# Kernel tuning notes

Hardware: AMD Instinct MI355X
Metric: run time of the kernel (lower is better)

Reference implementation:

```python
import jax, jax.numpy as jnp
import numpy as np

N_NODES = 50000
N_EDGES = 800000
IN_DIM = 128
HIDDEN = 32
HEADS = 4
OUT_DIM = 64
NEG_SLOPE = 0.2  # PyG GATConv default


def setup_inputs() -> dict:
    key = jax.random.key(0)
    ks = jax.random.split(key, 12)
    s = 0.05
    return {
        "x": jax.random.normal(ks[0], (N_NODES, IN_DIM), dtype=jnp.float32),
        "edge_index": jax.random.randint(ks[1], (2, N_EDGES), 0, N_NODES, dtype=jnp.int64),
        # layer 1: out = HEADS * HIDDEN, concat=True
        "W1": jax.random.normal(ks[2], (IN_DIM, HEADS * HIDDEN), dtype=jnp.float32) * s,
        "a_src1": jax.random.normal(ks[3], (HEADS, HIDDEN), dtype=jnp.float32) * s,
        "a_dst1": jax.random.normal(ks[4], (HEADS, HIDDEN), dtype=jnp.float32) * s,
        "b1": jnp.zeros((HEADS * HIDDEN,), dtype=jnp.float32),
        # layer 2: heads=1, concat=False
        "W2": jax.random.normal(ks[5], (HEADS * HIDDEN, OUT_DIM), dtype=jnp.float32) * s,
        "a_src2": jax.random.normal(ks[6], (1, OUT_DIM), dtype=jnp.float32) * s,
        "a_dst2": jax.random.normal(ks[7], (1, OUT_DIM), dtype=jnp.float32) * s,
        "b2": jnp.zeros((OUT_DIM,), dtype=jnp.float32),
    }


def _gat_conv(x, src, dst, W, a_src, a_dst, b, heads, concat):
    """PyG-style GATConv. src/dst already include self-loops."""
    N = x.shape[0]
    C = W.shape[1] // heads
    h = (x @ W).reshape(N, heads, C)              # [N,H,C]
    al_s = jnp.sum(h * a_src, axis=-1)            # [N,H]
    al_d = jnp.sum(h * a_dst, axis=-1)            # [N,H]
    e = jax.nn.leaky_relu(al_s[src] + al_d[dst], NEG_SLOPE)  # [E,H]
    # numerically-stable segment softmax over incoming edges of each dst node
    m = jax.ops.segment_max(e, dst, num_segments=N)          # [N,H]
    ex = jnp.exp(e - m[dst])
    denom = jax.ops.segment_sum(ex, dst, num_segments=N)     # [N,H]
    alpha = ex / denom[dst]                                   # [E,H]
    out = jax.ops.segment_sum(h[src] * alpha[:, :, None], dst, num_segments=N)  # [N,H,C]
    out = out.reshape(N, heads * C) if concat else out.mean(axis=1)
    return out + b


def reference(x, edge_index, W1, a_src1, a_dst1, b1, W2, a_src2, a_dst2, b2):
    N = x.shape[0]
    loop = jnp.arange(N, dtype=edge_index.dtype)
    src = jnp.concatenate([edge_index[0], loop])
    dst = jnp.concatenate([edge_index[1], loop])
    h = jax.nn.relu(_gat_conv(x, src, dst, W1, a_src1, a_dst1, b1, HEADS, True))
    out = _gat_conv(h, src, dst, W2, a_src2, a_dst2, b2, 1, False)
    return jax.nn.log_softmax(out, axis=1)
```

## Files before the change

### kernel.cpp

```cpp
#include <hip/hip_runtime.h>
#include <hip/hip_bf16.h>
#include <math.h>

#define N_NODES 50000
#define N_EDGES 800000
#define E_TOT   (N_EDGES + N_NODES)
#define IN_DIM  128
#define HID     128
#define ODIM    64
#define NEG     0.2f
#define NB1     ((N_NODES + 255) / 256)
#define NCHUNK  ((N_NODES + 31) / 32)
#define NREP    8

typedef short bf16x8 __attribute__((ext_vector_type(8)));
typedef float f32x4 __attribute__((ext_vector_type(4)));
typedef float f32x2 __attribute__((ext_vector_type(2)));
typedef unsigned short ushort_t;

__device__ __forceinline__ float lrelu(float x) { return x >= 0.f ? x : NEG * x; }

__device__ __forceinline__ unsigned short f2b(float v) {
  unsigned int b = __float_as_uint(v);
  b += 0x7fffu + ((b >> 16) & 1u);
  return (unsigned short)(b >> 16);
}
__device__ __forceinline__ float b2f(unsigned short u) {
  return __uint_as_float(((unsigned int)u) << 16);
}
__device__ __forceinline__ unsigned int f2b2(float lo, float hi) {
  union { __hip_bfloat162 h; unsigned int u; } cv;
  cv.h = __float22bfloat162_rn(make_float2(lo, hi));
  return cv.u;
}
__device__ __forceinline__ float blo(unsigned int v) { return __uint_as_float(v << 16); }
__device__ __forceinline__ float bhi(unsigned int v) { return __uint_as_float(v & 0xffff0000u); }

__device__ __forceinline__ f32x2 f8x2lo(unsigned int v) {
  return __builtin_amdgcn_cvt_pk_f32_fp8((int)v, false);
}
__device__ __forceinline__ f32x2 f8x2hi(unsigned int v) {
  return __builtin_amdgcn_cvt_pk_f32_fp8((int)v, true);
}
__device__ __forceinline__ unsigned char f2f8(float v) {
  return (unsigned char)(__builtin_amdgcn_cvt_pk_fp8_f32(v, v, 0, false) & 0xff);
}

__device__ __forceinline__ int e_src(const void* ei, int f, int e) {
  if (e >= N_EDGES) return e - N_EDGES;
  return f ? (int)((const long long*)ei)[e] : ((const int*)ei)[e];
}
__device__ __forceinline__ int e_dst(const void* ei, int f, int e) {
  if (e >= N_EDGES) return e - N_EDGES;
  return f ? (int)((const long long*)ei)[N_EDGES + e] : ((const int*)ei)[N_EDGES + e];
}

__global__ void k_prep(const float* __restrict__ W1, const float* __restrict__ W2,
                       ushort_t* __restrict__ Wt1, ushort_t* __restrict__ Wt2,
                       const void* ei, int* flag) {
  if (blockIdx.x == 64) {
    if (threadIdx.x == 0) {
      const int* p = (const int*)ei;
      int allz = 1;
      for (int i = 0; i < 64; ++i) if (p[2 * i + 1] != 0) { allz = 0; break; }
      *flag = allz;
    }
    return;
  }
  int i = blockIdx.x * 256 + threadIdx.x;
  if (i < 128 * 128) { int k = i >> 7, n = i & 127; Wt1[n * 128 + k] = f2b(W1[i]); }
  if (i < 128 * 64)  { int k = i >> 6, n = i & 63;  Wt2[n * 128 + k] = f2b(W2[i]); }
}

__global__ void k_hist(const void* ei, const int* flag, int* degr, int* rank) {
  int e = blockIdx.x * 256 + threadIdx.x;
  if (e >= E_TOT) return;
  int r = blockIdx.x & (NREP - 1);
  int d = e_dst(ei, *flag, e);
  rank[e] = atomicAdd(&degr[r * N_NODES + d], 1);
}

__global__ void k_scan1(const int* __restrict__ degr, int* __restrict__ offs, int* __restrict__ bsums) {
  __shared__ int sm[256];
  int t = threadIdx.x, i = blockIdx.x * 256 + t;
  int v = 0;
  if (i < N_NODES) {
    #pragma unroll
    for (int r = 0; r < NREP; ++r) v += degr[r * N_NODES + i];
  }
  sm[t] = v;
  __syncthreads();
  for (int o = 1; o < 256; o <<= 1) {
    int add = (t >= o) ? sm[t - o] : 0;
    __syncthreads();
    sm[t] += add;
    __syncthreads();
  }
  if (i < N_NODES) offs[i] = sm[t] - v;
  if (t == 255) bsums[blockIdx.x] = sm[255];
}

__global__ void k_scan2(int* bsums) {
  __shared__ int sm[256];
  int t = threadIdx.x;
  int v = (t < NB1) ? bsums[t] : 0;
  sm[t] = v;
  __syncthreads();
  for (int o = 1; o < 256; o <<= 1) {
    int add = (t >= o) ? sm[t - o] : 0;
    __syncthreads();
    sm[t] += add;
    __syncthreads();
  }
  if (t < NB1) bsums[t] = sm[t] - v;
}

__global__ void k_scan3(int* __restrict__ offs, const int* __restrict__ bsums,
                        const int* __restrict__ degr, int* __restrict__ repbase) {
  int i = blockIdx.x * 256 + threadIdx.x;
  if (i < N_NODES) {
    int o = offs[i] + bsums[blockIdx.x];
    offs[i] = o;
    int run = o;
    #pragma unroll
    for (int r = 0; r < NREP; ++r) {
      repbase[r * N_NODES + i] = run;
      run += degr[r * N_NODES + i];
    }
  }
  if (i == 0) offs[N_NODES] = E_TOT;
}

__global__ void k_scatter(const void* ei, const int* __restrict__ flag,
                          const int* __restrict__ repbase,
                          const int* __restrict__ rank, int* __restrict__ srcs) {
  int e = blockIdx.x * 256 + threadIdx.x;
  if (e >= E_TOT) return;
  int f = *flag;
  int d = e_dst(ei, f, e);
  int r = blockIdx.x & (NREP - 1);
  srcs[repbase[r * N_NODES + d] + rank[e]] = e_src(ei, f, e);
}

__global__ __launch_bounds__(256) void k_mm1(const float* __restrict__ x,
                                             const ushort_t* __restrict__ Wt,
                                             ushort_t* __restrict__ h1b,
                                             unsigned char* __restrict__ h1f8) {
  __shared__ ushort_t xs[32 * 128];
  int t = threadIdx.x;
  int w = t >> 6, l = t & 63;
  int lr = l & 15, lk = l >> 4;
  int nodeSub = (w & 1) * 16, colBase = (w >> 1) * 64;
  bf16x8 bfrag[4][4];
  #pragma unroll
  for (int ct = 0; ct < 4; ++ct)
    #pragma unroll
    for (int ks = 0; ks < 4; ++ks) {
      int n = colBase + ct * 16 + lr;
      int k = ks * 32 + lk * 8;
      bfrag[ct][ks] = *(const bf16x8*)&Wt[n * 128 + k];
    }
  int rr = t >> 3, c0 = (t & 7) * 16;
  for (int chunk = blockIdx.x; chunk < NCHUNK; chunk += gridDim.x) {
    int base = chunk * 32;
    int srcRow = base + rr; if (srcRow >= N_NODES) srcRow = N_NODES - 1;
    const float4* xr = (const float4*)&x[(size_t)srcRow * IN_DIM + c0];
    float4 f0 = xr[0], f1 = xr[1], f2 = xr[2], f3 = xr[3];
    uint4 w0, w1;
    w0.x = f2b2(f0.x, f0.y); w0.y = f2b2(f0.z, f0.w);
    w0.z = f2b2(f1.x, f1.y); w0.w = f2b2(f1.z, f1.w);
    w1.x = f2b2(f2.x, f2.y); w1.y = f2b2(f2.z, f2.w);
    w1.z = f2b2(f3.x, f3.y); w1.w = f2b2(f3.z, f3.w);
    char* xsb = (char*)xs;
    int swz = (rr & 7) << 4;
    *(uint4*)(xsb + rr * 256 + ((c0 * 2 +  0) ^ swz)) = w0;
    *(uint4*)(xsb + rr * 256 + ((c0 * 2 + 16) ^ swz)) = w1;
    __syncthreads();
    f32x4 acc[4] = {{0,0,0,0},{0,0,0,0},{0,0,0,0},{0,0,0,0}};
    int arow = nodeSub + lr;
    #pragma unroll
    for (int ks = 0; ks < 4; ++ks) {
      bf16x8 a = *(const bf16x8*)((const char*)xs + arow * 256 +
                                  ((ks * 64 + lk * 16) ^ ((arow & 7) << 4)));
      #pragma unroll
      for (int ct = 0; ct < 4; ++ct)
        acc[ct] = __builtin_amdgcn_mfma_f32_16x16x32_bf16(a, bfrag[ct][ks], acc[ct], 0, 0, 0);
    }
    __syncthreads();
    #pragma unroll
    for (int ct = 0; ct < 4; ++ct)
      #pragma unroll
      for (int r = 0; r < 4; ++r) {
        int node = base + nodeSub + lk * 4 + r;
        if (node < N_NODES) {
          float v = acc[ct][r];
          int col = colBase + ct * 16 + lr;
          h1b[(size_t)node * HID + col] = f2b(v);
          h1f8[(size_t)node * HID + col] = f2f8(v);
        }
      }
  }
}

__global__ __launch_bounds__(256) void k_mm2(const ushort_t* __restrict__ xb,
                                             const ushort_t* __restrict__ Wt,
                                             ushort_t* __restrict__ h2b,
                                             unsigned char* __restrict__ h2f8) {
  __shared__ ushort_t xs[32 * 128];
  int t = threadIdx.x;
  int w = t >> 6, l = t & 63;
  int lr = l & 15, lk = l >> 4;
  int nodeSub = (w & 1) * 16, colBase = (w >> 1) * 32;
  bf16x8 bfrag[2][4];
  #pragma unroll
  for (int ct = 0; ct < 2; ++ct)
    #pragma unroll
    for (int ks = 0; ks < 4; ++ks) {
      int n = colBase + ct * 16 + lr;
      int k = ks * 32 + lk * 8;
      bfrag[ct][ks] = *(const bf16x8*)&Wt[n * 128 + k];
    }
  int rr = t >> 3, c0 = (t & 7) * 16;
  for (int chunk = blockIdx.x; chunk < NCHUNK; chunk += gridDim.x) {
    int base = chunk * 32;
    int srcRow = base + rr; if (srcRow >= N_NODES) srcRow = N_NODES - 1;
    const uint4* xr = (const uint4*)&xb[(size_t)srcRow * HID + c0];
    uint4 w0 = xr[0], w1 = xr[1];
    char* xsb = (char*)xs;
    int swz = (rr & 7) << 4;
    *(uint4*)(xsb + rr * 256 + ((c0 * 2 +  0) ^ swz)) = w0;
    *(uint4*)(xsb + rr * 256 + ((c0 * 2 + 16) ^ swz)) = w1;
    __syncthreads();
    f32x4 acc[2] = {{0,0,0,0},{0,0,0,0}};
    int arow = nodeSub + lr;
    #pragma unroll
    for (int ks = 0; ks < 4; ++ks) {
      bf16x8 a = *(const bf16x8*)((const char*)xs + arow * 256 +
                                  ((ks * 64 + lk * 16) ^ ((arow & 7) << 4)));
      #pragma unroll
      for (int ct = 0; ct < 2; ++ct)
        acc[ct] = __builtin_amdgcn_mfma_f32_16x16x32_bf16(a, bfrag[ct][ks], acc[ct], 0, 0, 0);
    }
    __syncthreads();
    #pragma unroll
    for (int ct = 0; ct < 2; ++ct)
      #pragma unroll
      for (int r = 0; r < 4; ++r) {
        int node = base + nodeSub + lk * 4 + r;
        if (node < N_NODES) {
          float v = acc[ct][r];
          int col = colBase + ct * 16 + lr;
          h2b[(size_t)node * ODIM + col] = f2b(v);
          h2f8[(size_t)node * ODIM + col] = f2f8(v);
        }
      }
  }
}

__global__ __launch_bounds__(256) void k_al1(const ushort_t* __restrict__ h1b,
                                             const float* __restrict__ asrc,
                                             const float* __restrict__ adst, float* __restrict__ als,
                                             float* __restrict__ ald) {
  int t = threadIdx.x;
  int n = blockIdx.x * 16 + (t >> 4);
  int c8 = (t & 15) * 8;
  uint4 v = *(const uint4*)&h1b[(size_t)n * HID + c8];
  float4 a0 = *(const float4*)&asrc[c8], a1 = *(const float4*)&asrc[c8 + 4];
  float4 d0 = *(const float4*)&adst[c8], d1 = *(const float4*)&adst[c8 + 4];
  float f0 = blo(v.x), f1 = bhi(v.x), f2 = blo(v.y), f3 = bhi(v.y);
  float f4 = blo(v.z), f5 = bhi(v.z), f6 = blo(v.w), f7 = bhi(v.w);
  float s = f0*a0.x + f1*a0.y + f2*a0.z + f3*a0.w + f4*a1.x + f5*a1.y + f6*a1.z + f7*a1.w;
  float d = f0*d0.x + f1*d0.y + f2*d0.z + f3*d0.w + f4*d1.x + f5*d1.y + f6*d1.z + f7*d1.w;
  s += __shfl_xor(s, 1); s += __shfl_xor(s, 2);
  d += __shfl_xor(d, 1); d += __shfl_xor(d, 2);
  if ((t & 3) == 0) {
    int head = (t & 15) >> 2;
    als[n * 4 + head] = s;
    ald[n * 4 + head] = d;
  }
}

__global__ __launch_bounds__(256) void k_al2(const ushort_t* __restrict__ h2b,
                                             const float* __restrict__ asrc,
                                             const float* __restrict__ adst, float* __restrict__ als,
                                             float* __restrict__ ald) {
  int t = threadIdx.x;
  int n = blockIdx.x * 32 + (t >> 3);
  if (n >= N_NODES) return;
  int c8 = (t & 7) * 8;
  uint4 v = *(const uint4*)&h2b[(size_t)n * ODIM + c8];
  float4 a0 = *(const float4*)&asrc[c8], a1 = *(const float4*)&asrc[c8 + 4];
  float4 d0 = *(const float4*)&adst[c8], d1 = *(const float4*)&adst[c8 + 4];
  float f0 = blo(v.x), f1 = bhi(v.x), f2 = blo(v.y), f3 = bhi(v.y);
  float f4 = blo(v.z), f5 = bhi(v.z), f6 = blo(v.w), f7 = bhi(v.w);
  float s = f0*a0.x + f1*a0.y + f2*a0.z + f3*a0.w + f4*a1.x + f5*a1.y + f6*a1.z + f7*a1.w;
  float d = f0*d0.x + f1*d0.y + f2*d0.z + f3*d0.w + f4*d1.x + f5*d1.y + f6*d1.z + f7*d1.w;
  s += __shfl_xor(s, 1); s += __shfl_xor(s, 2); s += __shfl_xor(s, 4);
  d += __shfl_xor(d, 1); d += __shfl_xor(d, 2); d += __shfl_xor(d, 4);
  if ((t & 7) == 0) { als[n] = s; ald[n] = d; }
}

__global__ __launch_bounds__(256) void k_agg1(const unsigned char* __restrict__ h1f8,
                                              const float* __restrict__ als,
                                              const float* __restrict__ ald, const int* __restrict__ offs,
                                              const int* __restrict__ srcs, const float* __restrict__ b1,
                                              ushort_t* __restrict__ out1b) {
  int t = threadIdx.x;
  int w = t >> 6, l = t & 63;
  int hw = l >> 5, lh = l & 31;
  int sg = lh >> 4, cl = lh & 15, head = cl >> 2;
  int lbase = hw << 5;
  int n = blockIdx.x * 8 + w * 2 + hw;
  int off0 = offs[n], deg = offs[n + 1] - off0;
  const float4* als4 = (const float4*)als;
  float4 ad = ((const float4*)ald)[n];
  const unsigned char* hb = h1f8 + cl * 8;

  float ds = 0.f;
  float num0 = 0, num1 = 0, num2 = 0, num3 = 0, num4 = 0, num5 = 0, num6 = 0, num7 = 0;

  for (int cbase = 0; cbase < deg; cbase += 32) {
    int j0 = cbase + lh;
    float w0 = 0.f, w1 = 0.f, w2 = 0.f, w3 = 0.f;
    int sb = 0;
    if (j0 < deg) {
      int s = srcs[off0 + j0];
      sb = s << 7;
      float4 a = als4[s];
      w0 = __expf(lrelu(a.x + ad.x)); w1 = __expf(lrelu(a.y + ad.y));
      w2 = __expf(lrelu(a.z + ad.z)); w3 = __expf(lrelu(a.w + ad.w));
    }
    int pw01 = (int)f2b2(w0, w1), pw23 = (int)f2b2(w2, w3);
    int cn = (deg - cbase) < 32 ? (deg - cbase) : 32;
    for (int jj = 0; jj < cn; jj += 4) {
      int jA = jj + sg, jB = jj + 2 + sg;
      int boA = __shfl(sb, lbase + jA), boB = __shfl(sb, lbase + jB);
      uint2 vA = *(const uint2*)(hb + boA);
      uint2 vB = *(const uint2*)(hb + boB);
      unsigned int uA01 = (unsigned int)__shfl(pw01, lbase + jA);
      unsigned int uA23 = (unsigned int)__shfl(pw23, lbase + jA);
      unsigned int uB01 = (unsigned int)__shfl(pw01, lbase + jB);
      unsigned int uB23 = (unsigned int)__shfl(pw23, lbase + jB);
      unsigned int upA = head < 2 ? uA01 : uA23;
      unsigned int upB = head < 2 ? uB01 : uB23;
      float wA = (head & 1) ? bhi(upA) : blo(upA);
      float wB = (head & 1) ? bhi(upB) : blo(upB);
      ds += wA + wB;
      f32x2 p0 = f8x2lo(vA.x), p1 = f8x2hi(vA.x);
      f32x2 p2 = f8x2lo(vA.y), p3 = f8x2hi(vA.y);
      num0 = fmaf(wA, p0.x, num0); num1 = fmaf(wA, p0.y, num1);
      num2 = fmaf(wA, p1.x, num2); num3 = fmaf(wA, p1.y, num3);
      num4 = fmaf(wA, p2.x, num4); num5 = fmaf(wA, p2.y, num5);
      num6 = fmaf(wA, p3.x, num6); num7 = fmaf(wA, p3.y, num7);
      p0 = f8x2lo(vB.x); p1 = f8x2hi(vB.x);
      p2 = f8x2lo(vB.y); p3 = f8x2hi(vB.y);
      num0 = fmaf(wB, p0.x, num0); num1 = fmaf(wB, p0.y, num1);
      num2 = fmaf(wB, p1.x, num2); num3 = fmaf(wB, p1.y, num3);
      num4 = fmaf(wB, p2.x, num4); num5 = fmaf(wB, p2.y, num5);
      num6 = fmaf(wB, p3.x, num6); num7 = fmaf(wB, p3.y, num7);
    }
  }
  num0 += __shfl_xor(num0, 16); num1 += __shfl_xor(num1, 16);
  num2 += __shfl_xor(num2, 16); num3 += __shfl_xor(num3, 16);
  num4 += __shfl_xor(num4, 16); num5 += __shfl_xor(num5, 16);
  num6 += __shfl_xor(num6, 16); num7 += __shfl_xor(num7, 16);
  ds += __shfl_xor(ds, 16);
  if (lh < 16) {
    float rd = 1.f / ds;
    int c8 = cl * 8;
    float4 bb0 = *(const float4*)&b1[c8];
    float4 bb1 = *(const float4*)&b1[c8 + 4];
    float o0 = fmaxf(num0 * rd + bb0.x, 0.f);
    float o1 = fmaxf(num1 * rd + bb0.y, 0.f);
    float o2 = fmaxf(num2 * rd + bb0.z, 0.f);
    float o3 = fmaxf(num3 * rd + bb0.w, 0.f);
    float o4 = fmaxf(num4 * rd + bb1.x, 0.f);
    float o5 = fmaxf(num5 * rd + bb1.y, 0.f);
    float o6 = fmaxf(num6 * rd + bb1.z, 0.f);
    float o7 = fmaxf(num7 * rd + bb1.w, 0.f);
    uint4 pk;
    pk.x = f2b2(o0, o1); pk.y = f2b2(o2, o3);
    pk.z = f2b2(o4, o5); pk.w = f2b2(o6, o7);
    *(uint4*)&out1b[(size_t)n * HID + c8] = pk;
  }
}

__global__ __launch_bounds__(256) void k_agg2(const unsigned char* __restrict__ h2f8,
                                              const float* __restrict__ als,
                                              const float* __restrict__ ald, const int* __restrict__ offs,
                                              const int* __restrict__ srcs, const float* __restrict__ b2,
                                              float* __restrict__ out) {
  int t = threadIdx.x;
  int w = t >> 6, l = t & 63;
  int hw = l >> 5, lh = l & 31;
  int sg = lh >> 3, cl = lh & 7;
  int lbase = hw << 5;
  int n = blockIdx.x * 8 + w * 2 + hw;
  int off0 = offs[n], deg = offs[n + 1] - off0;
  float adv = ald[n];
  const unsigned char* hb = h2f8 + cl * 8;

  float ds = 0.f;
  float num0 = 0, num1 = 0, num2 = 0, num3 = 0, num4 = 0, num5 = 0, num6 = 0, num7 = 0;

  for (int cbase = 0; cbase < deg; cbase += 32) {
    int j0 = cbase + lh;
    float wv = 0.f;
    int sb = 0;
    if (j0 < deg) {
      int s = srcs[off0 + j0];
      sb = s << 6;
      wv = __expf(lrelu(als[s] + adv));
    }
    int cn = (deg - cbase) < 32 ? (deg - cbase) : 32;
    for (int jj = 0; jj < cn; jj += 8) {
      int jA = jj + sg, jB = jj + 4 + sg;
      int boA = __shfl(sb, lbase + jA), boB = __shfl(sb, lbase + jB);
      uint2 vA = *(const uint2*)(hb + boA);
      uint2 vB = *(const uint2*)(hb + boB);
      float wA = __shfl(wv, lbase + jA), wB = __shfl(wv, lbase + jB);
      ds += wA + wB;
      f32x2 p0 = f8x2lo(vA.x), p1 = f8x2hi(vA.x);
      f32x2 p2 = f8x2lo(vA.y), p3 = f8x2hi(vA.y);
      num0 = fmaf(wA, p0.x, num0); num1 = fmaf(wA, p0.y, num1);
      num2 = fmaf(wA, p1.x, num2); num3 = fmaf(wA, p1.y, num3);
      num4 = fmaf(wA, p2.x, num4); num5 = fmaf(wA, p2.y, num5);
      num6 = fmaf(wA, p3.x, num6); num7 = fmaf(wA, p3.y, num7);
      p0 = f8x2lo(vB.x); p1 = f8x2hi(vB.x);
      p2 = f8x2lo(vB.y); p3 = f8x2hi(vB.y);
      num0 = fmaf(wB, p0.x, num0); num1 = fmaf(wB, p0.y, num1);
      num2 = fmaf(wB, p1.x, num2); num3 = fmaf(wB, p1.y, num3);
      num4 = fmaf(wB, p2.x, num4); num5 = fmaf(wB, p2.y, num5);
      num6 = fmaf(wB, p3.x, num6); num7 = fmaf(wB, p3.y, num7);
    }
  }
  #pragma unroll
  for (int o = 8; o <= 16; o <<= 1) {
    num0 += __shfl_xor(num0, o); num1 += __shfl_xor(num1, o);
    num2 += __shfl_xor(num2, o); num3 += __shfl_xor(num3, o);
    num4 += __shfl_xor(num4, o); num5 += __shfl_xor(num5, o);
    num6 += __shfl_xor(num6, o); num7 += __shfl_xor(num7, o);
    ds += __shfl_xor(ds, o);
  }
  if (lh < 8) {
    float rd = 1.f / ds;
    int c8 = cl * 8;
    float4 bb0 = *(const float4*)&b2[c8];
    float4 bb1 = *(const float4*)&b2[c8 + 4];
    float v0 = num0 * rd + bb0.x, v1 = num1 * rd + bb0.y;
    float v2 = num2 * rd + bb0.z, v3 = num3 * rd + bb0.w;
    float v4 = num4 * rd + bb1.x, v5 = num5 * rd + bb1.y;
    float v6 = num6 * rd + bb1.z, v7 = num7 * rd + bb1.w;
    float mx = fmaxf(fmaxf(fmaxf(v0, v1), fmaxf(v2, v3)), fmaxf(fmaxf(v4, v5), fmaxf(v6, v7)));
    #pragma unroll
    for (int o = 1; o <= 4; o <<= 1) mx = fmaxf(mx, __shfl_xor(mx, o));
    float sum = __expf(v0 - mx) + __expf(v1 - mx) + __expf(v2 - mx) + __expf(v3 - mx)
              + __expf(v4 - mx) + __expf(v5 - mx) + __expf(v6 - mx) + __expf(v7 - mx);
    #pragma unroll
    for (int o = 1; o <= 4; o <<= 1) sum += __shfl_xor(sum, o);
    float ls = __logf(sum);
    float4 r0, r1;
    r0.x = (v0 - mx) - ls; r0.y = (v1 - mx) - ls; r0.z = (v2 - mx) - ls; r0.w = (v3 - mx) - ls;
    r1.x = (v4 - mx) - ls; r1.y = (v5 - mx) - ls; r1.z = (v6 - mx) - ls; r1.w = (v7 - mx) - ls;
    *(float4*)&out[(size_t)n * ODIM + c8] = r0;
    *(float4*)&out[(size_t)n * ODIM + c8 + 4] = r1;
  }
}

extern "C" void kernel_launch(void* const* d_in, const int* in_sizes, int n_in,
                              void* d_out, int out_size, void* d_ws, size_t ws_size,
                              hipStream_t stream) {
  const float* x   = (const float*)d_in[0];
  const void*  ei  = d_in[1];
  const float* W1  = (const float*)d_in[2];
  const float* as1 = (const float*)d_in[3];
  const float* ad1 = (const float*)d_in[4];
  const float* b1  = (const float*)d_in[5];
  const float* W2  = (const float*)d_in[6];
  const float* as2 = (const float*)d_in[7];
  const float* ad2 = (const float*)d_in[8];
  const float* b2  = (const float*)d_in[9];
  float* out = (float*)d_out;

  char* ws = (char*)d_ws;
  size_t o = 0;
  auto alloc = [&](size_t bytes) { void* p = (void*)(ws + o); o += (bytes + 255) & ~(size_t)255; return p; };
  ushort_t* h1b   = (ushort_t*)alloc((size_t)N_NODES * HID * 2);
  ushort_t* out1b = (ushort_t*)alloc((size_t)N_NODES * HID * 2);
  ushort_t* h2b   = (ushort_t*)alloc((size_t)N_NODES * ODIM * 2);
  unsigned char* h1f8 = (unsigned char*)alloc((size_t)N_NODES * HID);
  ushort_t* Wt1   = (ushort_t*)alloc((size_t)128 * 128 * 2);
  ushort_t* Wt2   = (ushort_t*)alloc((size_t)64 * 128 * 2);
  float* als1 = (float*)alloc((size_t)N_NODES * 4 * 4);
  float* ald1 = (float*)alloc((size_t)N_NODES * 4 * 4);
  float* als2 = (float*)alloc((size_t)N_NODES * 4);
  float* ald2 = (float*)alloc((size_t)N_NODES * 4);
  int*   degr = (int*)alloc((size_t)NREP * N_NODES * 4);
  int*   repbase = (int*)alloc((size_t)NREP * N_NODES * 4);
  int*   offs = (int*)alloc((size_t)(N_NODES + 1) * 4);
  int*   rank = (int*)alloc((size_t)E_TOT * 4);
  int*   srcs = (int*)alloc((size_t)E_TOT * 4);
  int*   bsums= (int*)alloc((size_t)NB1 * 4);
  int*   flag = (int*)alloc(4);
  unsigned char* h2f8 = (unsigned char*)rank;

  hipMemsetAsync(degr, 0, (size_t)NREP * N_NODES * 4, stream);
  k_prep   <<<65,    256, 0, stream>>>(W1, W2, Wt1, Wt2, ei, flag);

  int egrid = (E_TOT + 255) / 256;
  k_hist   <<<egrid, 256, 0, stream>>>(ei, flag, degr, rank);
  k_scan1  <<<NB1,   256, 0, stream>>>(degr, offs, bsums);
  k_scan2  <<<1,     256, 0, stream>>>(bsums);
  k_scan3  <<<NB1,   256, 0, stream>>>(offs, bsums, degr, repbase);
  k_scatter<<<egrid, 256, 0, stream>>>(ei, flag, repbase, rank, srcs);

  k_mm1  <<<512, 256, 0, stream>>>(x, Wt1, h1b, h1f8);
  k_al1  <<<N_NODES / 16, 256, 0, stream>>>(h1b, as1, ad1, als1, ald1);
  k_agg1 <<<N_NODES / 8, 256, 0, stream>>>(h1f8, als1, ald1, offs, srcs, b1, out1b);

  k_mm2  <<<512, 256, 0, stream>>>(out1b, Wt2, h2b, h2f8);
  k_al2  <<<(N_NODES + 31) / 32, 256, 0, stream>>>(h2b, as2, ad2, als2, ald2);
  k_agg2 <<<N_NODES / 8, 256, 0, stream>>>(h2f8, als2, ald2, offs, srcs, b2, out);
}
```

Measured before the change: 134.3 us.

## Fold memset and scan2 into neighbours; drop shuffle staging in aggregation kernels

The degree-array memset moves into extra blocks of the prep kernel, and the single-block scan2 is removed by having each scan3 block reduce the preceding block sums itself. This cuts two launches from the serial chain. Both aggregation kernels also drop the cooperative load-then-shuffle scheme: each lane now loads its own source index and per-head attention logit and computes the exp weight directly. This removes the shuffles and bf16 weight packing but repeats the index loads and exp work across lanes.

```diff
diff --git a/kernel.cpp b/kernel.cpp
--- a/kernel.cpp
+++ b/kernel.cpp
@@ -57,7 +57,7 @@
 
 __global__ void k_prep(const float* __restrict__ W1, const float* __restrict__ W2,
                        ushort_t* __restrict__ Wt1, ushort_t* __restrict__ Wt2,
-                       const void* ei, int* flag) {
+                       const void* ei, int* flag, int4* __restrict__ degr4) {
   if (blockIdx.x == 64) {
     if (threadIdx.x == 0) {
       const int* p = (const int*)ei;
@@ -67,6 +67,11 @@
     }
     return;
   }
+  if (blockIdx.x > 64) {
+    int i = (blockIdx.x - 65) * 256 + threadIdx.x;
+    if (i < NREP * N_NODES / 4) degr4[i] = make_int4(0, 0, 0, 0);
+    return;
+  }
   int i = blockIdx.x * 256 + threadIdx.x;
   if (i < 128 * 128) { int k = i >> 7, n = i & 127; Wt1[n * 128 + k] = f2b(W1[i]); }
   if (i < 128 * 64)  { int k = i >> 6, n = i & 63;  Wt2[n * 128 + k] = f2b(W2[i]); }
@@ -100,26 +105,19 @@
   if (t == 255) bsums[blockIdx.x] = sm[255];
 }
 
-__global__ void k_scan2(int* bsums) {
-  __shared__ int sm[256];
-  int t = threadIdx.x;
-  int v = (t < NB1) ? bsums[t] : 0;
-  sm[t] = v;
-  __syncthreads();
-  for (int o = 1; o < 256; o <<= 1) {
-    int add = (t >= o) ? sm[t - o] : 0;
-    __syncthreads();
-    sm[t] += add;
-    __syncthreads();
-  }
-  if (t < NB1) bsums[t] = sm[t] - v;
-}
-
 __global__ void k_scan3(int* __restrict__ offs, const int* __restrict__ bsums,
                         const int* __restrict__ degr, int* __restrict__ repbase) {
-  int i = blockIdx.x * 256 + threadIdx.x;
+  __shared__ int red[4];
+  int t = threadIdx.x;
+  int v = (t < blockIdx.x) ? bsums[t] : 0;
+  #pragma unroll
+  for (int o = 32; o >= 1; o >>= 1) v += __shfl_xor(v, o);
+  if ((t & 63) == 0) red[t >> 6] = v;
+  __syncthreads();
+  int pre = red[0] + red[1] + red[2] + red[3];
+  int i = blockIdx.x * 256 + t;
   if (i < N_NODES) {
-    int o = offs[i] + bsums[blockIdx.x];
+    int o = offs[i] + pre;
     offs[i] = o;
     int run = o;
     #pragma unroll
@@ -309,56 +307,50 @@
   int w = t >> 6, l = t & 63;
   int hw = l >> 5, lh = l & 31;
   int sg = lh >> 4, cl = lh & 15, head = cl >> 2;
-  int lbase = hw << 5;
   int n = blockIdx.x * 8 + w * 2 + hw;
   int off0 = offs[n], deg = offs[n + 1] - off0;
-  const float4* als4 = (const float4*)als;
-  float4 ad = ((const float4*)ald)[n];
+  float adh = ald[n * 4 + head];
   const unsigned char* hb = h1f8 + cl * 8;
 
   float ds = 0.f;
   float num0 = 0, num1 = 0, num2 = 0, num3 = 0, num4 = 0, num5 = 0, num6 = 0, num7 = 0;
 
-  for (int cbase = 0; cbase < deg; cbase += 32) {
-    int j0 = cbase + lh;
-    float w0 = 0.f, w1 = 0.f, w2 = 0.f, w3 = 0.f;
-    int sb = 0;
-    if (j0 < deg) {
-      int s = srcs[off0 + j0];
-      sb = s << 7;
-      float4 a = als4[s];
-      w0 = __expf(lrelu(a.x + ad.x)); w1 = __expf(lrelu(a.y + ad.y));
-      w2 = __expf(lrelu(a.z + ad.z)); w3 = __expf(lrelu(a.w + ad.w));
-    }
-    int pw01 = (int)f2b2(w0, w1), pw23 = (int)f2b2(w2, w3);
-    int cn = (deg - cbase) < 32 ? (deg - cbase) : 32;
-    for (int jj = 0; jj < cn; jj += 4) {
-      int jA = jj + sg, jB = jj + 2 + sg;
-      int boA = __shfl(sb, lbase + jA), boB = __shfl(sb, lbase + jB);
-      uint2 vA = *(const uint2*)(hb + boA);
-      uint2 vB = *(const uint2*)(hb + boB);
-      unsigned int uA01 = (unsigned int)__shfl(pw01, lbase + jA);
-      unsigned int uA23 = (unsigned int)__shfl(pw23, lbase + jA);
-      unsigned int uB01 = (unsigned int)__shfl(pw01, lbase + jB);
-      unsigned int uB23 = (unsigned int)__shfl(pw23, lbase + jB);
-      unsigned int upA = head < 2 ? uA01 : uA23;
-      unsigned int upB = head < 2 ? uB01 : uB23;
-      float wA = (head & 1) ? bhi(upA) : blo(upA);
-      float wB = (head & 1) ? bhi(upB) : blo(upB);
-      ds += wA + wB;
-      f32x2 p0 = f8x2lo(vA.x), p1 = f8x2hi(vA.x);
-      f32x2 p2 = f8x2lo(vA.y), p3 = f8x2hi(vA.y);
-      num0 = fmaf(wA, p0.x, num0); num1 = fmaf(wA, p0.y, num1);
-      num2 = fmaf(wA, p1.x, num2); num3 = fmaf(wA, p1.y, num3);
-      num4 = fmaf(wA, p2.x, num4); num5 = fmaf(wA, p2.y, num5);
-      num6 = fmaf(wA, p3.x, num6); num7 = fmaf(wA, p3.y, num7);
-      p0 = f8x2lo(vB.x); p1 = f8x2hi(vB.x);
-      p2 = f8x2lo(vB.y); p3 = f8x2hi(vB.y);
-      num0 = fmaf(wB, p0.x, num0); num1 = fmaf(wB, p0.y, num1);
-      num2 = fmaf(wB, p1.x, num2); num3 = fmaf(wB, p1.y, num3);
-      num4 = fmaf(wB, p2.x, num4); num5 = fmaf(wB, p2.y, num5);
-      num6 = fmaf(wB, p3.x, num6); num7 = fmaf(wB, p3.y, num7);
-    }
+  int j = sg;
+  for (; j + 2 < deg; j += 4) {
+    int sA = srcs[off0 + j];
+    int sB = srcs[off0 + j + 2];
+    float aA = als[sA * 4 + head];
+    float aB = als[sB * 4 + head];
+    uint2 vA = *(const uint2*)(hb + (sA << 7));
+    uint2 vB = *(const uint2*)(hb + (sB << 7));
+    float wA = __expf(lrelu(aA + adh));
+    float wB = __expf(lrelu(aB + adh));
+    ds += wA + wB;
+    f32x2 p0 = f8x2lo(vA.x), p1 = f8x2hi(vA.x);
+    f32x2 p2 = f8x2lo(vA.y), p3 = f8x2hi(vA.y);
+    num0 = fmaf(wA, p0.x, num0); num1 = fmaf(wA, p0.y, num1);
+    num2 = fmaf(wA, p1.x, num2); num3 = fmaf(wA, p1.y, num3);
+    num4 = fmaf(wA, p2.x, num4); num5 = fmaf(wA, p2.y, num5);
+    num6 = fmaf(wA, p3.x, num6); num7 = fmaf(wA, p3.y, num7);
+    p0 = f8x2lo(vB.x); p1 = f8x2hi(vB.x);
+    p2 = f8x2lo(vB.y); p3 = f8x2hi(vB.y);
+    num0 = fmaf(wB, p0.x, num0); num1 = fmaf(wB, p0.y, num1);
+    num2 = fmaf(wB, p1.x, num2); num3 = fmaf(wB, p1.y, num3);
+    num4 = fmaf(wB, p2.x, num4); num5 = fmaf(wB, p2.y, num5);
+    num6 = fmaf(wB, p3.x, num6); num7 = fmaf(wB, p3.y, num7);
+  }
+  if (j < deg) {
+    int sA = srcs[off0 + j];
+    float aA = als[sA * 4 + head];
+    uint2 vA = *(const uint2*)(hb + (sA << 7));
+    float wA = __expf(lrelu(aA + adh));
+    ds += wA;
+    f32x2 p0 = f8x2lo(vA.x), p1 = f8x2hi(vA.x);
+    f32x2 p2 = f8x2lo(vA.y), p3 = f8x2hi(vA.y);
+    num0 = fmaf(wA, p0.x, num0); num1 = fmaf(wA, p0.y, num1);
+    num2 = fmaf(wA, p1.x, num2); num3 = fmaf(wA, p1.y, num3);
+    num4 = fmaf(wA, p2.x, num4); num5 = fmaf(wA, p2.y, num5);
+    num6 = fmaf(wA, p3.x, num6); num7 = fmaf(wA, p3.y, num7);
   }
   num0 += __shfl_xor(num0, 16); num1 += __shfl_xor(num1, 16);
   num2 += __shfl_xor(num2, 16); num3 += __shfl_xor(num3, 16);
@@ -394,7 +386,6 @@
   int w = t >> 6, l = t & 63;
   int hw = l >> 5, lh = l & 31;
   int sg = lh >> 3, cl = lh & 7;
-  int lbase = hw << 5;
   int n = blockIdx.x * 8 + w * 2 + hw;
   int off0 = offs[n], deg = offs[n + 1] - off0;
   float adv = ald[n];
@@ -403,36 +394,42 @@
   float ds = 0.f;
   float num0 = 0, num1 = 0, num2 = 0, num3 = 0, num4 = 0, num5 = 0, num6 = 0, num7 = 0;
 
-  for (int cbase = 0; cbase < deg; cbase += 32) {
-    int j0 = cbase + lh;
-    float wv = 0.f;
-    int sb = 0;
-    if (j0 < deg) {
-      int s = srcs[off0 + j0];
-      sb = s << 6;
-      wv = __expf(lrelu(als[s] + adv));
-    }
-    int cn = (deg - cbase) < 32 ? (deg - cbase) : 32;
-    for (int jj = 0; jj < cn; jj += 8) {
-      int jA = jj + sg, jB = jj + 4 + sg;
-      int boA = __shfl(sb, lbase + jA), boB = __shfl(sb, lbase + jB);
-      uint2 vA = *(const uint2*)(hb + boA);
-      uint2 vB = *(const uint2*)(hb + boB);
-      float wA = __shfl(wv, lbase + jA), wB = __shfl(wv, lbase + jB);
-      ds += wA + wB;
-      f32x2 p0 = f8x2lo(vA.x), p1 = f8x2hi(vA.x);
-      f32x2 p2 = f8x2lo(vA.y), p3 = f8x2hi(vA.y);
-      num0 = fmaf(wA, p0.x, num0); num1 = fmaf(wA, p0.y, num1);
-      num2 = fmaf(wA, p1.x, num2); num3 = fmaf(wA, p1.y, num3);
-      num4 = fmaf(wA, p2.x, num4); num5 = fmaf(wA, p2.y, num5);
-      num6 = fmaf(wA, p3.x, num6); num7 = fmaf(wA, p3.y, num7);
-      p0 = f8x2lo(vB.x); p1 = f8x2hi(vB.x);
-      p2 = f8x2lo(vB.y); p3 = f8x2hi(vB.y);
-      num0 = fmaf(wB, p0.x, num0); num1 = fmaf(wB, p0.y, num1);
-      num2 = fmaf(wB, p1.x, num2); num3 = fmaf(wB, p1.y, num3);
-      num4 = fmaf(wB, p2.x, num4); num5 = fmaf(wB, p2.y, num5);
-      num6 = fmaf(wB, p3.x, num6); num7 = fmaf(wB, p3.y, num7);
-    }
+  int j = sg;
+  for (; j + 4 < deg; j += 8) {
+    int sA = srcs[off0 + j];
+    int sB = srcs[off0 + j + 4];
+    float aA = als[sA];
+    float aB = als[sB];
+    uint2 vA = *(const uint2*)(hb + (sA << 6));
+    uint2 vB = *(const uint2*)(hb + (sB << 6));
+    float wA = __expf(lrelu(aA + adv));
+    float wB = __expf(lrelu(aB + adv));
+    ds += wA + wB;
+    f32x2 p0 = f8x2lo(vA.x), p1 = f8x2hi(vA.x);
+    f32x2 p2 = f8x2lo(vA.y), p3 = f8x2hi(vA.y);
+    num0 = fmaf(wA, p0.x, num0); num1 = fmaf(wA, p0.y, num1);
+    num2 = fmaf(wA, p1.x, num2); num3 = fmaf(wA, p1.y, num3);
+    num4 = fmaf(wA, p2.x, num4); num5 = fmaf(wA, p2.y, num5);
+    num6 = fmaf(wA, p3.x, num6); num7 = fmaf(wA, p3.y, num7);
+    p0 = f8x2lo(vB.x); p1 = f8x2hi(vB.x);
+    p2 = f8x2lo(vB.y); p3 = f8x2hi(vB.y);
+    num0 = fmaf(wB, p0.x, num0); num1 = fmaf(wB, p0.y, num1);
+    num2 = fmaf(wB, p1.x, num2); num3 = fmaf(wB, p1.y, num3);
+    num4 = fmaf(wB, p2.x, num4); num5 = fmaf(wB, p2.y, num5);
+    num6 = fmaf(wB, p3.x, num6); num7 = fmaf(wB, p3.y, num7);
+  }
+  if (j < deg) {
+    int sA = srcs[off0 + j];
+    float aA = als[sA];
+    uint2 vA = *(const uint2*)(hb + (sA << 6));
+    float wA = __expf(lrelu(aA + adv));
+    ds += wA;
+    f32x2 p0 = f8x2lo(vA.x), p1 = f8x2hi(vA.x);
+    f32x2 p2 = f8x2lo(vA.y), p3 = f8x2hi(vA.y);
+    num0 = fmaf(wA, p0.x, num0); num1 = fmaf(wA, p0.y, num1);
+    num2 = fmaf(wA, p1.x, num2); num3 = fmaf(wA, p1.y, num3);
+    num4 = fmaf(wA, p2.x, num4); num5 = fmaf(wA, p2.y, num5);
+    num6 = fmaf(wA, p3.x, num6); num7 = fmaf(wA, p3.y, num7);
   }
   #pragma unroll
   for (int o = 8; o <= 16; o <<= 1) {
@@ -504,13 +501,12 @@
   int*   flag = (int*)alloc(4);
   unsigned char* h2f8 = (unsigned char*)rank;
 
-  hipMemsetAsync(degr, 0, (size_t)NREP * N_NODES * 4, stream);
-  k_prep   <<<65,    256, 0, stream>>>(W1, W2, Wt1, Wt2, ei, flag);
+  int prepGrid = 65 + (NREP * N_NODES / 4 + 255) / 256;
+  k_prep   <<<prepGrid, 256, 0, stream>>>(W1, W2, Wt1, Wt2, ei, flag, (int4*)degr);
 
   int egrid = (E_TOT + 255) / 256;
   k_hist   <<<egrid, 256, 0, stream>>>(ei, flag, degr, rank);
   k_scan1  <<<NB1,   256, 0, stream>>>(degr, offs, bsums);
-  k_scan2  <<<1,     256, 0, stream>>>(bsums);
   k_scan3  <<<NB1,   256, 0, stream>>>(offs, bsums, degr, repbase);
   k_scatter<<<egrid, 256, 0, stream>>>(ei, flag, repbase, rank, srcs);
 
```

After: 133.3 us. About the same (-0.7%).
